# Performance work log

Hardware: AMD Instinct MI355X
Metric: run time of the kernel (lower is better)

The kernel has to match this reference:

```python
import jax, jax.numpy as jnp
import numpy as np
import math

B, S, D, H = 2048, 32, 1024, 16
DK = D // H
EPS = 1e-5

def setup_inputs() -> dict:
    key = jax.random.key(0)
    ks = jax.random.split(key, 8)
    w_scale = 0.02  # realistic init scale for linear weights
    # Weights stored as (d_in, d_out): y = x @ W + b (same math as torch x @ W.T)
    return {
        "x":  jax.random.normal(ks[0], (B, S, D), jnp.float32),
        "ln_g": jnp.ones((D,), jnp.float32),
        "ln_b": jnp.zeros((D,), jnp.float32),
        "wq": jax.random.normal(ks[1], (D, D), jnp.float32) * w_scale,
        "bq": jnp.zeros((D,), jnp.float32),
        "wk": jax.random.normal(ks[2], (D, D), jnp.float32) * w_scale,
        "bk": jnp.zeros((D,), jnp.float32),
        "wv": jax.random.normal(ks[3], (D, D), jnp.float32) * w_scale,
        "bv": jnp.zeros((D,), jnp.float32),
        "wo": jax.random.normal(ks[4], (D, D), jnp.float32) * w_scale,
        "bo": jnp.zeros((D,), jnp.float32),
        "rel_bias": jax.random.normal(ks[5], (H, 32, 32), jnp.float32),
    }

def reference(x, ln_g, ln_b, wq, bq, wk, bk, wv, bv, wo, bo, rel_bias):
    b, s, d = x.shape
    h = rel_bias.shape[0]
    dk = d // h
    residual = x
    # LayerNorm (eps=1e-5)
    mu = jnp.mean(x, axis=-1, keepdims=True)
    var = jnp.mean(jnp.square(x - mu), axis=-1, keepdims=True)
    xn = (x - mu) * jax.lax.rsqrt(var + EPS) * ln_g + ln_b
    # QKV projections -> [b, h, s, dk]
    def split_heads(t):
        return t.reshape(b, s, h, dk).transpose(0, 2, 1, 3)
    Q = split_heads(xn @ wq + bq)
    K = split_heads(xn @ wk + bk)
    V = split_heads(xn @ wv + bv)
    scores = jnp.einsum('bhqd,bhkd->bhqk', Q, K) / jnp.sqrt(jnp.float32(dk))
    if s <= 32:  # static at trace time, matching the torch branch
        scores = scores + rel_bias[:, :s, :s][None]
    attn = jax.nn.softmax(scores, axis=-1)
    ctx = jnp.einsum('bhqk,bhkd->bhqd', attn, V)
    ctx = ctx.transpose(0, 2, 1, 3).reshape(b, s, d)
    out = ctx @ wo + bo  # dropout is identity in eval
    return residual + out
```

## Files before the change

### kernel.cpp

```cpp
#include <hip/hip_runtime.h>
#include <stdint.h>


typedef __attribute__((ext_vector_type(8))) short bf16x8;
typedef __attribute__((ext_vector_type(4))) float f32x4;
typedef __attribute__((ext_vector_type(16))) float f32x16;

__device__ __forceinline__ float bf2f(unsigned short u) {
    return __uint_as_float(((unsigned)u) << 16);
}
__device__ __forceinline__ unsigned short f2bf(float f) {
    unsigned u = __float_as_uint(f);
    u += 0x7FFFu + ((u >> 16) & 1u);
    return (unsigned short)(u >> 16);
}
__device__ __forceinline__ uint4 pack8(const float* f) {
    uint4 u;
    u.x = (unsigned)f2bf(f[0]) | ((unsigned)f2bf(f[1]) << 16);
    u.y = (unsigned)f2bf(f[2]) | ((unsigned)f2bf(f[3]) << 16);
    u.z = (unsigned)f2bf(f[4]) | ((unsigned)f2bf(f[5]) << 16);
    u.w = (unsigned)f2bf(f[6]) | ((unsigned)f2bf(f[7]) << 16);
    return u;
}

typedef __attribute__((address_space(3))) unsigned lds_u32;
typedef const __attribute__((address_space(1))) unsigned glb_u32;
__device__ __forceinline__ void gld16(const void* g, void* l) {
    __builtin_amdgcn_global_load_lds((glb_u32*)g, (lds_u32*)l, 16, 0, 0);
}

__global__ __launch_bounds__(256) void transpose_w(
    const float* __restrict__ wq, const float* __restrict__ wk,
    const float* __restrict__ wv, const float* __restrict__ wo,
    unsigned short* __restrict__ wcatT, unsigned short* __restrict__ woT)
{
    __shared__ unsigned short T[64 * 72];
    int bid = blockIdx.x;
    int p = bid >> 8;
    int t = bid & 255;
    int k0 = (t >> 4) * 64, n0 = (t & 15) * 64;
    const float* src = (p == 0) ? wq : (p == 1) ? wk : (p == 2) ? wv : wo;
    unsigned short* dst = (p < 3) ? (wcatT + (size_t)p * 1048576) : woT;
    int tid = threadIdx.x;
#pragma unroll
    for (int it = 0; it < 2; it++) {
        int flat = it * 2048 + tid * 8;
        int r = flat >> 6, c = flat & 63;
        const float* s4 = src + (size_t)(k0 + r) * 1024 + n0 + c;
        float4 u0 = *(const float4*)s4;
        float4 u1 = *(const float4*)(s4 + 4);
        float f[8] = {u0.x, u0.y, u0.z, u0.w, u1.x, u1.y, u1.z, u1.w};
        *(uint4*)&T[r * 72 + c] = pack8(f);
    }
    __syncthreads();
#pragma unroll
    for (int it = 0; it < 2; it++) {
        int flat = it * 2048 + tid * 8;
        int rn = flat >> 6, ck = flat & 63;
        unsigned short v[8];
#pragma unroll
        for (int j = 0; j < 8; j++) v[j] = T[(ck + j) * 72 + rn];
        uint4 u;
        u.x = (unsigned)v[0] | ((unsigned)v[1] << 16);
        u.y = (unsigned)v[2] | ((unsigned)v[3] << 16);
        u.z = (unsigned)v[4] | ((unsigned)v[5] << 16);
        u.w = (unsigned)v[6] | ((unsigned)v[7] << 16);
        *(uint4*)(dst + (size_t)(n0 + rn) * 1024 + k0 + ck) = u;
    }
}

__global__ __launch_bounds__(256) void ln_kernel(
    const float* __restrict__ x, const float* __restrict__ gg,
    const float* __restrict__ bb, unsigned short* __restrict__ xn)
{
    int l = threadIdx.x & 63;
    size_t row = (size_t)blockIdx.x * 4 + (threadIdx.x >> 6);
    const float* xr = x + row * 1024;
    float f0[8], f1[8];
    *(float4*)&f0[0] = *(const float4*)(xr + l * 8);
    *(float4*)&f0[4] = *(const float4*)(xr + l * 8 + 4);
    *(float4*)&f1[0] = *(const float4*)(xr + 512 + l * 8);
    *(float4*)&f1[4] = *(const float4*)(xr + 512 + l * 8 + 4);
    float s = 0.f, s2 = 0.f;
#pragma unroll
    for (int j = 0; j < 8; j++) { s += f0[j] + f1[j]; s2 += f0[j] * f0[j] + f1[j] * f1[j]; }
#pragma unroll
    for (int m = 1; m < 64; m <<= 1) { s += __shfl_xor(s, m); s2 += __shfl_xor(s2, m); }
    float mu = s * (1.f / 1024.f);
    float var = s2 * (1.f / 1024.f) - mu * mu;
    float rs = rsqrtf(var + 1e-5f);
    float fg0[8], fg1[8], fb0[8], fb1[8];
    *(float4*)&fg0[0] = *(const float4*)(gg + l * 8);
    *(float4*)&fg0[4] = *(const float4*)(gg + l * 8 + 4);
    *(float4*)&fg1[0] = *(const float4*)(gg + 512 + l * 8);
    *(float4*)&fg1[4] = *(const float4*)(gg + 512 + l * 8 + 4);
    *(float4*)&fb0[0] = *(const float4*)(bb + l * 8);
    *(float4*)&fb0[4] = *(const float4*)(bb + l * 8 + 4);
    *(float4*)&fb1[0] = *(const float4*)(bb + 512 + l * 8);
    *(float4*)&fb1[4] = *(const float4*)(bb + 512 + l * 8 + 4);
    float o0[8], o1[8];
#pragma unroll
    for (int j = 0; j < 8; j++) {
        o0[j] = (f0[j] - mu) * rs * fg0[j] + fb0[j];
        o1[j] = (f1[j] - mu) * rs * fg1[j] + fb1[j];
    }
    *(uint4*)(xn + row * 1024 + l * 8) = pack8(o0);
    *(uint4*)(xn + row * 1024 + 512 + l * 8) = pack8(o1);
}

#define FENCE asm volatile("" ::: "memory")
#define BARRIER do { FENCE; __builtin_amdgcn_s_barrier(); FENCE; } while (0)
#define WAIT_LGKM0 do { asm volatile("s_waitcnt lgkmcnt(0)" ::: "memory"); \
                        __builtin_amdgcn_sched_barrier(0); } while (0)
#define VMCNT(n) asm volatile("s_waitcnt vmcnt(" #n ")" ::: "memory")

#define SAp(buf) (LDSU + (buf) * 16384)
#define SBp(buf) (LDSU + 32768 + (buf) * 16384)

#define STG(gb, h, kcol, ldsreg) do { \
    const unsigned short* _g = (gb) + (size_t)((h) * 128) * 1024 + (kcol); \
    unsigned short* _d = (ldsreg) + ((h) * 128 + w * 8) * 64; \
    gld16(_g, _d); gld16(_g + 64 * 1024, _d + 64 * 64); } while (0)

#define LDA(buf, q, rfq, ks) (*(const bf16x8*)&SAp(buf)[ \
    (wm * 128 + (q) * 32 + (rfq) * 16 + (l & 15)) * 64 + ((((ks) * 32) + khi) ^ aswz)])
#define LDB(buf, cf, ks) (*(const bf16x8*)&SBp(buf)[ \
    (wn * 64 + (cf) * 16 + (l & 15)) * 64 + ((((ks) * 32) + khi) ^ aswz)])

#define MFMA_QUAD(q) do { \
    _Pragma("unroll") \
    for (int cf = 0; cf < 4; cf++) { \
        acc[(q)*2+0][cf] = __builtin_amdgcn_mfma_f32_16x16x32_bf16(aF00, bF[cf][0], acc[(q)*2+0][cf], 0, 0, 0); \
        acc[(q)*2+0][cf] = __builtin_amdgcn_mfma_f32_16x16x32_bf16(aF01, bF[cf][1], acc[(q)*2+0][cf], 0, 0, 0); \
        acc[(q)*2+1][cf] = __builtin_amdgcn_mfma_f32_16x16x32_bf16(aF10, bF[cf][0], acc[(q)*2+1][cf], 0, 0, 0); \
        acc[(q)*2+1][cf] = __builtin_amdgcn_mfma_f32_16x16x32_bf16(aF11, bF[cf][1], acc[(q)*2+1][cf], 0, 0, 0); \
    } } while (0)

#define PHASE(buf, q, STAGE_STMT, TAIL_STMT) do { \
    bf16x8 aF00 = LDA(buf, q, 0, 0), aF01 = LDA(buf, q, 0, 1); \
    bf16x8 aF10 = LDA(buf, q, 1, 0), aF11 = LDA(buf, q, 1, 1); \
    if ((q) == 0) { \
        _Pragma("unroll") \
        for (int cf = 0; cf < 4; cf++) { bF[cf][0] = LDB(buf, cf, 0); bF[cf][1] = LDB(buf, cf, 1); } \
    } \
    STAGE_STMT; \
    BARRIER; \
    WAIT_LGKM0; \
    __builtin_amdgcn_s_setprio(1); \
    MFMA_QUAD(q); \
    __builtin_amdgcn_s_setprio(0); \
    TAIL_STMT; \
    BARRIER; \
} while (0)

template <int MODE>
__global__ __launch_bounds__(512, 2) void gemm8(
    const unsigned short* __restrict__ A, const unsigned short* __restrict__ Bt,
    const float* __restrict__ bz0, const float* __restrict__ bz1,
    const float* __restrict__ bz2, const float* __restrict__ resid,
    void* __restrict__ outv, int NTL, size_t pstride)
{
    __shared__ __align__(16) unsigned short LDSU[65536];
    int cpx = gridDim.x >> 3;
    int bid = (blockIdx.x & 7) * cpx + (blockIdx.x >> 3);
    int mt = bid / NTL, ntl = bid % NTL;
    int m0 = mt * 256, n0 = ntl * 256;
    int tid = threadIdx.x, l = tid & 63, w = tid >> 6;
    int wm = w >> 2, wn = w & 3;
    int khi = (l >> 4) * 8;
    int aswz = (l & 7) * 8;

    const unsigned short* Ag = A + (size_t)(m0 + w * 8 + (l >> 3)) * 1024 + ((l & 7) ^ (l >> 3)) * 8;
    const unsigned short* Bg = Bt + (size_t)(n0 + w * 8 + (l >> 3)) * 1024 + ((l & 7) ^ (l >> 3)) * 8;
    unsigned short* sA0 = SAp(0);
    unsigned short* sA1 = SAp(1);
    unsigned short* sB0 = SBp(0);
    unsigned short* sB1 = SBp(1);

    f32x4 acc[8][4];
#pragma unroll
    for (int i = 0; i < 8; i++)
#pragma unroll
        for (int j = 0; j < 4; j++)
#pragma unroll
            for (int v = 0; v < 4; v++) acc[i][j][v] = 0.f;

    bf16x8 bF[4][2];

    STG(Ag, 0, 0, sA0); STG(Ag, 1, 0, sA0);
    STG(Bg, 0, 0, sB0); STG(Bg, 1, 0, sB0);
    STG(Bg, 0, 64, sB1); STG(Bg, 1, 64, sB1);
    VMCNT(4);
    BARRIER;

    for (int it = 0; it < 7; ++it) {
        int koff = it * 128;
        PHASE(0, 0, STG(Ag, 0, koff + 64, sA1), (void)0);
        PHASE(0, 1, STG(Ag, 1, koff + 64, sA1), (void)0);
        PHASE(0, 2, STG(Bg, 0, koff + 128, sB0), (void)0);
        PHASE(0, 3, STG(Bg, 1, koff + 128, sB0), VMCNT(4));
        PHASE(1, 0, STG(Ag, 0, koff + 128, sA0), (void)0);
        PHASE(1, 1, STG(Ag, 1, koff + 128, sA0), (void)0);
        PHASE(1, 2, STG(Bg, 0, koff + 192, sB1), (void)0);
        PHASE(1, 3, STG(Bg, 1, koff + 192, sB1), VMCNT(4));
    }
    PHASE(0, 0, STG(Ag, 0, 960, sA1), (void)0);
    PHASE(0, 1, STG(Ag, 1, 960, sA1), (void)0);
    PHASE(0, 2, (void)0, (void)0);
    PHASE(0, 3, (void)0, VMCNT(0));
    PHASE(1, 0, (void)0, (void)0);
    PHASE(1, 1, (void)0, (void)0);
    PHASE(1, 2, (void)0, (void)0);
    PHASE(1, 3, (void)0, (void)0);
    __builtin_amdgcn_sched_barrier(0);

    if (MODE == 0) {
        unsigned short* Cs = LDSU;
        unsigned short* out = (unsigned short*)outv;
        int p = n0 >> 10;
        const float* bp = (p == 0) ? bz0 : (p == 1) ? bz1 : bz2;
        size_t pbase = (size_t)p * pstride;
        __syncthreads();
#pragma unroll
        for (int cf = 0; cf < 4; cf++) {
            int colc = wn * 64 + cf * 16 + (l & 15);
            int nn = ((n0 + colc) & 1023);
            float bias = bp[nn];
            int c8 = colc >> 3, ce = colc & 7;
#pragma unroll
            for (int rf = 0; rf < 8; rf++) {
#pragma unroll
                for (int v = 0; v < 4; v++) {
                    int rloc = wm * 128 + rf * 16 + (l >> 4) * 4 + v;
                    Cs[rloc * 256 + ((c8 ^ (rloc & 7)) << 3) + ce] =
                        f2bf(acc[rf][cf][v] + bias);
                }
            }
        }
        __syncthreads();
        int bg0 = m0 >> 5;
        int hg0 = (n0 & 1023) >> 6;
#pragma unroll
        for (int k = 0; k < 4; k++) {
            int pi = w * 4 + k;
            int b = pi >> 2, hh = pi & 3;
#pragma unroll
            for (int r4 = 0; r4 < 4; r4++) {
                int c = r4 * 64 + l;
                int s = c >> 3, d8 = c & 7;
                int row = b * 32 + s;
                int c8 = hh * 8 + d8;
                uint4 val = *(const uint4*)&Cs[row * 256 + ((c8 ^ (row & 7)) << 3)];
                size_t dst = pbase + (((size_t)((bg0 + b) * 16 + hg0 + hh) * 32 + s) << 6) + d8 * 8;
                *(uint4*)(out + dst) = val;
            }
        }
    } else {
        float* Cf = (float*)LDSU;
        float* out = (float*)outv;
        int gcol = n0 + l * 4;
        float4 bzv = *(const float4*)(bz0 + gcol);
#pragma unroll
        for (int pass = 0; pass < 2; pass++) {
            __syncthreads();
#pragma unroll
            for (int rfq = 0; rfq < 4; rfq++) {
                int rf = pass * 4 + rfq;
#pragma unroll
                for (int cf = 0; cf < 4; cf++) {
                    int c0 = wn * 64 + cf * 16 + (l & 15);
                    int c4 = c0 >> 2, ce = c0 & 3;
#pragma unroll
                    for (int v = 0; v < 4; v++) {
                        int rl = wm * 64 + rfq * 16 + (l >> 4) * 4 + v;
                        Cf[rl * 256 + ((c4 ^ (rl & 7)) << 2) + ce] = acc[rf][cf][v];
                    }
                }
            }
            __syncthreads();
#pragma unroll
            for (int rb4 = 0; rb4 < 4; rb4++) {
                float4 rz[4], cv[4];
#pragma unroll
                for (int k = 0; k < 4; k++) {
                    int rr = (rb4 * 4 + k) * 8 + w;
                    int grow = m0 + (rr & 63) + ((rr >> 6) << 7) + pass * 64;
                    rz[k] = *(const float4*)(resid + (size_t)grow * 1024 + gcol);
                }
#pragma unroll
                for (int k = 0; k < 4; k++) {
                    int rr = (rb4 * 4 + k) * 8 + w;
                    cv[k] = *(const float4*)&Cf[rr * 256 + ((l ^ (rr & 7)) << 2)];
                }
#pragma unroll
                for (int k = 0; k < 4; k++) {
                    int rr = (rb4 * 4 + k) * 8 + w;
                    int grow = m0 + (rr & 63) + ((rr >> 6) << 7) + pass * 64;
                    float4 o;
                    o.x = cv[k].x + bzv.x + rz[k].x;
                    o.y = cv[k].y + bzv.y + rz[k].y;
                    o.z = cv[k].z + bzv.z + rz[k].z;
                    o.w = cv[k].w + bzv.w + rz[k].w;
                    *(float4*)(out + (size_t)grow * 1024 + gcol) = o;
                }
            }
        }
    }
}

__global__ __launch_bounds__(512) void attn_kernel(
    const unsigned short* __restrict__ qkv, const float* __restrict__ rb,
    unsigned short* __restrict__ ctx, size_t pstride)
{
    __shared__ unsigned short VT[8][64 * 40];
    __shared__ unsigned short Ps[8][32 * 40];
    int w8 = threadIdx.x >> 6, l = threadIdx.x & 63;
    int col = l & 31, hi = l >> 5;
    int bh = blockIdx.x * 8 + w8, h = bh & 15;
    size_t base = (size_t)bh << 11;
    const unsigned short* Qb = qkv + base;
    const unsigned short* Kb = Qb + pstride;
    const unsigned short* Vb = Kb + pstride;
    unsigned short* vt = VT[w8];
    unsigned short* ps = Ps[w8];

#pragma unroll
    for (int r = 0; r < 4; r++) {
        int flat = r * 512 + l * 8;
        int s = flat >> 6, d0 = flat & 63;
        uint4 u = *(const uint4*)(Vb + flat);
        const unsigned short* e = (const unsigned short*)&u;
#pragma unroll
        for (int j = 0; j < 8; j++) vt[(d0 + j) * 40 + s] = e[j];
    }

    f32x16 acc;
#pragma unroll
    for (int i = 0; i < 16; i++) acc[i] = 0.f;
#pragma unroll
    for (int t = 0; t < 4; t++) {
        bf16x8 aQ = *(const bf16x8*)(Qb + col * 64 + t * 16 + hi * 8);
        bf16x8 bK = *(const bf16x8*)(Kb + col * 64 + t * 16 + hi * 8);
        acc = __builtin_amdgcn_mfma_f32_32x32x16_bf16(aQ, bK, acc, 0, 0, 0);
    }

    const float* rbh = rb + h * 1024;
#pragma unroll
    for (int r = 0; r < 16; r++) {
        int m = (r & 3) + 8 * (r >> 2) + 4 * hi;
        float v = acc[r] * 0.125f + rbh[m * 32 + col];
        float mx = v;
#pragma unroll
        for (int msk = 1; msk < 32; msk <<= 1) mx = fmaxf(mx, __shfl_xor(mx, msk));
        float e = __expf(v - mx);
        float sm = e;
#pragma unroll
        for (int msk = 1; msk < 32; msk <<= 1) sm += __shfl_xor(sm, msk);
        ps[m * 40 + col] = f2bf(e / sm);
    }

    bf16x8 pa0 = *(const bf16x8*)&ps[(l & 31) * 40 + hi * 8];
    bf16x8 pa1 = *(const bf16x8*)&ps[(l & 31) * 40 + 16 + hi * 8];
    size_t rowb = (size_t)(bh >> 4) * 32;
#pragma unroll
    for (int c2 = 0; c2 < 2; c2++) {
        bf16x8 vb0 = *(const bf16x8*)&vt[(c2 * 32 + (l & 31)) * 40 + hi * 8];
        bf16x8 vb1 = *(const bf16x8*)&vt[(c2 * 32 + (l & 31)) * 40 + 16 + hi * 8];
        f32x16 o;
#pragma unroll
        for (int i = 0; i < 16; i++) o[i] = 0.f;
        o = __builtin_amdgcn_mfma_f32_32x32x16_bf16(pa0, vb0, o, 0, 0, 0);
        o = __builtin_amdgcn_mfma_f32_32x32x16_bf16(pa1, vb1, o, 0, 0, 0);
#pragma unroll
        for (int r = 0; r < 16; r++) {
            int m = (r & 3) + 8 * (r >> 2) + 4 * hi;
            ctx[(rowb + m) * 1024 + h * 64 + c2 * 32 + col] = f2bf(o[r]);
        }
    }
}

extern "C" void kernel_launch(void* const* d_in, const int* in_sizes, int n_in,
                              void* d_out, int out_size, void* d_ws, size_t ws_size,
                              hipStream_t stream)
{
    const float* x  = (const float*)d_in[0];
    const float* lg = (const float*)d_in[1];
    const float* lb = (const float*)d_in[2];
    const float* wq = (const float*)d_in[3];
    const float* bq = (const float*)d_in[4];
    const float* wk = (const float*)d_in[5];
    const float* bk = (const float*)d_in[6];
    const float* wv = (const float*)d_in[7];
    const float* bv = (const float*)d_in[8];
    const float* wo = (const float*)d_in[9];
    const float* bo = (const float*)d_in[10];
    const float* rb = (const float*)d_in[11];
    float* out = (float*)d_out;
    unsigned short* ws = (unsigned short*)d_ws;

    unsigned short* wcatT = ws;
    unsigned short* woT   = wcatT + 3145728;
    unsigned short* xnctx = woT + 1048576;
    unsigned short* qkvc  = xnctx + 67108864ull;

    const size_t elems_fixed = 3145728ull + 1048576ull + 67108864ull;
    const size_t need1 = (elems_fixed + 201326592ull) * 2;
    const size_t need4 = (elems_fixed + 50331648ull) * 2;
    int nChunks = (ws_size >= need1) ? 1 : (ws_size >= need4) ? 4 : 8;
    int rowsPer = 65536 / nChunks;
    size_t pstr = (size_t)rowsPer * 1024;

    transpose_w<<<dim3(1024), dim3(256), 0, stream>>>(wq, wk, wv, wo, wcatT, woT);
    ln_kernel<<<dim3(16384), dim3(256), 0, stream>>>(x, lg, lb, xnctx);

    int gemm0Grid = (rowsPer / 256) * 12;
    int attnGrid  = rowsPer / 16;

    for (int c = 0; c < nChunks; c++) {
        const unsigned short* Ac = xnctx + (size_t)c * pstr;
        unsigned short* ctxc = xnctx + (size_t)c * pstr;
        gemm8<0><<<dim3(gemm0Grid), dim3(512), 0, stream>>>(
            Ac, wcatT, bq, bk, bv, (const float*)nullptr, (void*)qkvc, 12, pstr);
        attn_kernel<<<dim3(attnGrid), dim3(512), 0, stream>>>(qkvc, rb, ctxc, pstr);
    }

    gemm8<1><<<dim3(1024), dim3(512), 0, stream>>>(
        xnctx, woT, bo, bo, bo, x, (void*)out, 4, 0);
}
```

Baseline: 785.0 us.

## Fuse QKV projection with per-head attention in one kernel

Replaces the chunked QKV GEMM plus separate attention kernel with one fused kernel. Each block computes a 256-row by 192-column tile (Q, K, V for one head), writes it to LDS with bias, and runs the 32x32 attention per wave directly from LDS. This removes the global round-trip of the QKV intermediate and the chunking logic. In exchange it uses a less efficient 256x192 GEMM tile at one block per CU because of the larger LDS footprint, and xn now re-reads the A tile for every head.

Result: no change. 782.1 us (-0.4%).

```diff
diff --git a/kernel.cpp b/kernel.cpp
--- a/kernel.cpp
+++ b/kernel.cpp
@@ -114,12 +114,180 @@
                         __builtin_amdgcn_sched_barrier(0); } while (0)
 #define VMCNT(n) asm volatile("s_waitcnt vmcnt(" #n ")" ::: "memory")
 
+#define FQ_SA(buf) (LDSU + (buf) * 16384)
+#define FQ_SB(buf) (LDSU + 32768 + (buf) * 12288)
+#define QS_OFF 0
+#define KS_OFF 18432
+#define VT_OFF 36864
+#define PS_OFF 57344
+
+#define ASTG(buf, g, koff) gld16(Ag + (size_t)(g) * 65536 + (koff), FQ_SA(buf) + ((g) * 64 + w * 8) * 64)
+#define BSTG(buf, p, koff) gld16(((p) == 0 ? Bgq : (p) == 1 ? Bgk : Bgv) + (koff), \
+                                 FQ_SB(buf) + ((p) * 64 + w * 8) * 64)
+
+#define FLDA(buf, q, rfq, ks) (*(const bf16x8*)&FQ_SA(buf)[ \
+    (wm * 128 + (q) * 32 + (rfq) * 16 + (l & 15)) * 64 + ((((ks) * 32) + khi) ^ aswz)])
+#define FLDB(buf, cf, ks) (*(const bf16x8*)&FQ_SB(buf)[ \
+    (wn * 48 + (cf) * 16 + (l & 15)) * 64 + ((((ks) * 32) + khi) ^ aswz)])
+
+#define MFMA_TRI(q) do { \
+    _Pragma("unroll") \
+    for (int cf = 0; cf < 3; cf++) { \
+        acc[(q)*2+0][cf] = __builtin_amdgcn_mfma_f32_16x16x32_bf16(aF00, bF[cf][0], acc[(q)*2+0][cf], 0, 0, 0); \
+        acc[(q)*2+0][cf] = __builtin_amdgcn_mfma_f32_16x16x32_bf16(aF01, bF[cf][1], acc[(q)*2+0][cf], 0, 0, 0); \
+        acc[(q)*2+1][cf] = __builtin_amdgcn_mfma_f32_16x16x32_bf16(aF10, bF[cf][0], acc[(q)*2+1][cf], 0, 0, 0); \
+        acc[(q)*2+1][cf] = __builtin_amdgcn_mfma_f32_16x16x32_bf16(aF11, bF[cf][1], acc[(q)*2+1][cf], 0, 0, 0); \
+    } } while (0)
+
+#define FPHASE(buf, q, STAGE_STMT, TAIL_STMT) do { \
+    bf16x8 aF00 = FLDA(buf, q, 0, 0), aF01 = FLDA(buf, q, 0, 1); \
+    bf16x8 aF10 = FLDA(buf, q, 1, 0), aF11 = FLDA(buf, q, 1, 1); \
+    if ((q) == 0) { \
+        _Pragma("unroll") \
+        for (int cf = 0; cf < 3; cf++) { bF[cf][0] = FLDB(buf, cf, 0); bF[cf][1] = FLDB(buf, cf, 1); } \
+    } \
+    STAGE_STMT; \
+    BARRIER; \
+    WAIT_LGKM0; \
+    __builtin_amdgcn_s_setprio(1); \
+    MFMA_TRI(q); \
+    __builtin_amdgcn_s_setprio(0); \
+    TAIL_STMT; \
+    BARRIER; \
+} while (0)
+
+__global__ __launch_bounds__(512, 1) void fqa_kernel(
+    const unsigned short* __restrict__ A, const unsigned short* __restrict__ wcatT,
+    const float* __restrict__ bq, const float* __restrict__ bk,
+    const float* __restrict__ bv, const float* __restrict__ rb,
+    unsigned short* __restrict__ ctx)
+{
+    __shared__ __align__(16) unsigned short LDSU[67584];
+    int cpx = gridDim.x >> 3;
+    int bid = (blockIdx.x & 7) * cpx + (blockIdx.x >> 3);
+    int mp = bid >> 4, h = bid & 15;
+    int m0 = mp * 256;
+    int tid = threadIdx.x, l = tid & 63, w = tid >> 6;
+    int wm = w >> 2, wn = w & 3;
+    int khi = (l >> 4) * 8;
+    int aswz = (l & 7) * 8;
+    int swzc = ((l & 7) ^ (l >> 3)) * 8;
+
+    const unsigned short* Ag  = A + (size_t)(m0 + w * 8 + (l >> 3)) * 1024 + swzc;
+    const unsigned short* Bgq = wcatT + (size_t)(h * 64 + w * 8 + (l >> 3)) * 1024 + swzc;
+    const unsigned short* Bgk = Bgq + 1048576ull;
+    const unsigned short* Bgv = Bgq + 2097152ull;
+
+    f32x4 acc[8][3];
+#pragma unroll
+    for (int i = 0; i < 8; i++)
+#pragma unroll
+        for (int j = 0; j < 3; j++)
+#pragma unroll
+            for (int v = 0; v < 4; v++) acc[i][j][v] = 0.f;
+
+    bf16x8 bF[3][2];
+
+    ASTG(0, 0, 0); ASTG(0, 1, 0); ASTG(0, 2, 0); ASTG(0, 3, 0);
+    BSTG(0, 0, 0); BSTG(0, 1, 0); BSTG(0, 2, 0);
+    BSTG(1, 0, 64); BSTG(1, 1, 64); BSTG(1, 2, 64);
+    VMCNT(3);
+    BARRIER;
+
+    for (int it = 0; it < 7; ++it) {
+        int ko1 = (2 * it + 1) * 64, ko2 = (2 * it + 2) * 64, ko3 = (2 * it + 3) * 64;
+        FPHASE(0, 0, do { ASTG(1, 0, ko1); ASTG(1, 1, ko1); } while (0), (void)0);
+        FPHASE(0, 1, do { ASTG(1, 2, ko1); ASTG(1, 3, ko1); } while (0), (void)0);
+        FPHASE(0, 2, do { BSTG(0, 0, ko2); BSTG(0, 1, ko2); } while (0), (void)0);
+        FPHASE(0, 3, BSTG(0, 2, ko2), VMCNT(3));
+        FPHASE(1, 0, do { ASTG(0, 0, ko2); ASTG(0, 1, ko2); } while (0), (void)0);
+        FPHASE(1, 1, do { ASTG(0, 2, ko2); ASTG(0, 3, ko2); } while (0), (void)0);
+        FPHASE(1, 2, do { BSTG(1, 0, ko3); BSTG(1, 1, ko3); } while (0), (void)0);
+        FPHASE(1, 3, BSTG(1, 2, ko3), VMCNT(3));
+    }
+    FPHASE(0, 0, do { ASTG(1, 0, 960); ASTG(1, 1, 960); } while (0), (void)0);
+    FPHASE(0, 1, do { ASTG(1, 2, 960); ASTG(1, 3, 960); } while (0), (void)0);
+    FPHASE(0, 2, (void)0, (void)0);
+    FPHASE(0, 3, (void)0, VMCNT(0));
+    FPHASE(1, 0, (void)0, (void)0);
+    FPHASE(1, 1, (void)0, (void)0);
+    FPHASE(1, 2, (void)0, (void)0);
+    FPHASE(1, 3, (void)0, (void)0);
+    __builtin_amdgcn_sched_barrier(0);
+
+#pragma unroll
+    for (int cf = 0; cf < 3; cf++) {
+        int seg = (wn * 3 + cf) >> 2;
+        int cseg = wn * 48 + cf * 16 + (l & 15) - (seg << 6);
+        const float* bp = (seg == 0) ? bq : (seg == 1) ? bk : bv;
+        float bias = bp[h * 64 + cseg];
+#pragma unroll
+        for (int ai = 0; ai < 8; ai++) {
+#pragma unroll
+            for (int v = 0; v < 4; v++) {
+                int row = wm * 128 + ai * 16 + (l >> 4) * 4 + v;
+                unsigned short val = f2bf(acc[ai][cf][v] + bias);
+                if (seg == 0)      LDSU[QS_OFF + row * 72 + cseg] = val;
+                else if (seg == 1) LDSU[KS_OFF + row * 72 + cseg] = val;
+                else               LDSU[VT_OFF + (((row >> 5) << 6) + cseg) * 40 + (row & 31)] = val;
+            }
+        }
+    }
+    __syncthreads();
+
+    {
+        int col = l & 31, hi = l >> 5;
+        f32x16 s;
+#pragma unroll
+        for (int i = 0; i < 16; i++) s[i] = 0.f;
+#pragma unroll
+        for (int t = 0; t < 4; t++) {
+            bf16x8 aQ = *(const bf16x8*)&LDSU[QS_OFF + (w * 32 + col) * 72 + t * 16 + hi * 8];
+            bf16x8 bK = *(const bf16x8*)&LDSU[KS_OFF + (w * 32 + col) * 72 + t * 16 + hi * 8];
+            s = __builtin_amdgcn_mfma_f32_32x32x16_bf16(aQ, bK, s, 0, 0, 0);
+        }
+        const float* rbh = rb + h * 1024;
+        unsigned short* ps = LDSU + PS_OFF + w * 1280;
+#pragma unroll
+        for (int r = 0; r < 16; r++) {
+            int m = (r & 3) + 8 * (r >> 2) + 4 * hi;
+            float v = s[r] * 0.125f + rbh[m * 32 + col];
+            float mx = v;
+#pragma unroll
+            for (int msk = 1; msk < 32; msk <<= 1) mx = fmaxf(mx, __shfl_xor(mx, msk));
+            float e = __expf(v - mx);
+            float sm = e;
+#pragma unroll
+            for (int msk = 1; msk < 32; msk <<= 1) sm += __shfl_xor(sm, msk);
+            ps[m * 40 + col] = f2bf(e / sm);
+        }
+        bf16x8 pa0 = *(const bf16x8*)&ps[col * 40 + hi * 8];
+        bf16x8 pa1 = *(const bf16x8*)&ps[col * 40 + 16 + hi * 8];
+        size_t rowb = ((size_t)mp * 8 + w) * 32;
+#pragma unroll
+        for (int c2 = 0; c2 < 2; c2++) {
+            bf16x8 vb0 = *(const bf16x8*)&LDSU[VT_OFF + (w * 64 + c2 * 32 + col) * 40 + hi * 8];
+            bf16x8 vb1 = *(const bf16x8*)&LDSU[VT_OFF + (w * 64 + c2 * 32 + col) * 40 + 16 + hi * 8];
+            f32x16 o;
+#pragma unroll
+            for (int i = 0; i < 16; i++) o[i] = 0.f;
+            o = __builtin_amdgcn_mfma_f32_32x32x16_bf16(pa0, vb0, o, 0, 0, 0);
+            o = __builtin_amdgcn_mfma_f32_32x32x16_bf16(pa1, vb1, o, 0, 0, 0);
+#pragma unroll
+            for (int r = 0; r < 16; r++) {
+                int m = (r & 3) + 8 * (r >> 2) + 4 * hi;
+                ctx[(rowb + m) * 1024 + h * 64 + c2 * 32 + col] = f2bf(o[r]);
+            }
+        }
+    }
+}
+
 #define SAp(buf) (LDSU + (buf) * 16384)
 #define SBp(buf) (LDSU + 32768 + (buf) * 16384)
 
-#define STG(gb, h, kcol, ldsreg) do { \
-    const unsigned short* _g = (gb) + (size_t)((h) * 128) * 1024 + (kcol); \
-    unsigned short* _d = (ldsreg) + ((h) * 128 + w * 8) * 64; \
+#define STG(gb, hh, kcol, ldsreg) do { \
+    const unsigned short* _g = (gb) + (size_t)((hh) * 128) * 1024 + (kcol); \
+    unsigned short* _d = (ldsreg) + ((hh) * 128 + w * 8) * 64; \
     gld16(_g, _d); gld16(_g + 64 * 1024, _d + 64 * 64); } while (0)
 
 #define LDA(buf, q, rfq, ks) (*(const bf16x8*)&SAp(buf)[ \
@@ -153,12 +321,10 @@
     BARRIER; \
 } while (0)
 
-template <int MODE>
-__global__ __launch_bounds__(512, 2) void gemm8(
+__global__ __launch_bounds__(512, 2) void gemm8res(
     const unsigned short* __restrict__ A, const unsigned short* __restrict__ Bt,
-    const float* __restrict__ bz0, const float* __restrict__ bz1,
-    const float* __restrict__ bz2, const float* __restrict__ resid,
-    void* __restrict__ outv, int NTL, size_t pstride)
+    const float* __restrict__ bz0, const float* __restrict__ resid,
+    float* __restrict__ out, int NTL)
 {
     __shared__ __align__(16) unsigned short LDSU[65536];
     int cpx = gridDim.x >> 3;
@@ -214,167 +380,52 @@
     PHASE(1, 3, (void)0, (void)0);
     __builtin_amdgcn_sched_barrier(0);
 
-    if (MODE == 0) {
-        unsigned short* Cs = LDSU;
-        unsigned short* out = (unsigned short*)outv;
-        int p = n0 >> 10;
-        const float* bp = (p == 0) ? bz0 : (p == 1) ? bz1 : bz2;
-        size_t pbase = (size_t)p * pstride;
+    float* Cf = (float*)LDSU;
+    int gcol = n0 + l * 4;
+    float4 bzv = *(const float4*)(bz0 + gcol);
+#pragma unroll
+    for (int pass = 0; pass < 2; pass++) {
         __syncthreads();
 #pragma unroll
-        for (int cf = 0; cf < 4; cf++) {
-            int colc = wn * 64 + cf * 16 + (l & 15);
-            int nn = ((n0 + colc) & 1023);
-            float bias = bp[nn];
-            int c8 = colc >> 3, ce = colc & 7;
-#pragma unroll
-            for (int rf = 0; rf < 8; rf++) {
+        for (int rfq = 0; rfq < 4; rfq++) {
+            int rf = pass * 4 + rfq;
+#pragma unroll
+            for (int cf = 0; cf < 4; cf++) {
+                int c0 = wn * 64 + cf * 16 + (l & 15);
+                int c4 = c0 >> 2, ce = c0 & 3;
 #pragma unroll
                 for (int v = 0; v < 4; v++) {
-                    int rloc = wm * 128 + rf * 16 + (l >> 4) * 4 + v;
-                    Cs[rloc * 256 + ((c8 ^ (rloc & 7)) << 3) + ce] =
-                        f2bf(acc[rf][cf][v] + bias);
+                    int rl = wm * 64 + rfq * 16 + (l >> 4) * 4 + v;
+                    Cf[rl * 256 + ((c4 ^ (rl & 7)) << 2) + ce] = acc[rf][cf][v];
                 }
             }
         }
         __syncthreads();
-        int bg0 = m0 >> 5;
-        int hg0 = (n0 & 1023) >> 6;
-#pragma unroll
-        for (int k = 0; k < 4; k++) {
-            int pi = w * 4 + k;
-            int b = pi >> 2, hh = pi & 3;
-#pragma unroll
-            for (int r4 = 0; r4 < 4; r4++) {
-                int c = r4 * 64 + l;
-                int s = c >> 3, d8 = c & 7;
-                int row = b * 32 + s;
-                int c8 = hh * 8 + d8;
-                uint4 val = *(const uint4*)&Cs[row * 256 + ((c8 ^ (row & 7)) << 3)];
-                size_t dst = pbase + (((size_t)((bg0 + b) * 16 + hg0 + hh) * 32 + s) << 6) + d8 * 8;
-                *(uint4*)(out + dst) = val;
-            }
-        }
-    } else {
-        float* Cf = (float*)LDSU;
-        float* out = (float*)outv;
-        int gcol = n0 + l * 4;
-        float4 bzv = *(const float4*)(bz0 + gcol);
-#pragma unroll
-        for (int pass = 0; pass < 2; pass++) {
-            __syncthreads();
-#pragma unroll
-            for (int rfq = 0; rfq < 4; rfq++) {
-                int rf = pass * 4 + rfq;
-#pragma unroll
-                for (int cf = 0; cf < 4; cf++) {
-                    int c0 = wn * 64 + cf * 16 + (l & 15);
-                    int c4 = c0 >> 2, ce = c0 & 3;
-#pragma unroll
-                    for (int v = 0; v < 4; v++) {
-                        int rl = wm * 64 + rfq * 16 + (l >> 4) * 4 + v;
-                        Cf[rl * 256 + ((c4 ^ (rl & 7)) << 2) + ce] = acc[rf][cf][v];
-                    }
-                }
-            }
-            __syncthreads();
-#pragma unroll
-            for (int rb4 = 0; rb4 < 4; rb4++) {
-                float4 rz[4], cv[4];
-#pragma unroll
-                for (int k = 0; k < 4; k++) {
-                    int rr = (rb4 * 4 + k) * 8 + w;
-                    int grow = m0 + (rr & 63) + ((rr >> 6) << 7) + pass * 64;
-                    rz[k] = *(const float4*)(resid + (size_t)grow * 1024 + gcol);
-                }
-#pragma unroll
-                for (int k = 0; k < 4; k++) {
-                    int rr = (rb4 * 4 + k) * 8 + w;
-                    cv[k] = *(const float4*)&Cf[rr * 256 + ((l ^ (rr & 7)) << 2)];
-                }
-#pragma unroll
-                for (int k = 0; k < 4; k++) {
-                    int rr = (rb4 * 4 + k) * 8 + w;
-                    int grow = m0 + (rr & 63) + ((rr >> 6) << 7) + pass * 64;
-                    float4 o;
-                    o.x = cv[k].x + bzv.x + rz[k].x;
-                    o.y = cv[k].y + bzv.y + rz[k].y;
-                    o.z = cv[k].z + bzv.z + rz[k].z;
-                    o.w = cv[k].w + bzv.w + rz[k].w;
-                    *(float4*)(out + (size_t)grow * 1024 + gcol) = o;
-                }
-            }
-        }
-    }
-}
-
-__global__ __launch_bounds__(512) void attn_kernel(
-    const unsigned short* __restrict__ qkv, const float* __restrict__ rb,
-    unsigned short* __restrict__ ctx, size_t pstride)
-{
-    __shared__ unsigned short VT[8][64 * 40];
-    __shared__ unsigned short Ps[8][32 * 40];
-    int w8 = threadIdx.x >> 6, l = threadIdx.x & 63;
-    int col = l & 31, hi = l >> 5;
-    int bh = blockIdx.x * 8 + w8, h = bh & 15;
-    size_t base = (size_t)bh << 11;
-    const unsigned short* Qb = qkv + base;
-    const unsigned short* Kb = Qb + pstride;
-    const unsigned short* Vb = Kb + pstride;
-    unsigned short* vt = VT[w8];
-    unsigned short* ps = Ps[w8];
-
-#pragma unroll
-    for (int r = 0; r < 4; r++) {
-        int flat = r * 512 + l * 8;
-        int s = flat >> 6, d0 = flat & 63;
-        uint4 u = *(const uint4*)(Vb + flat);
-        const unsigned short* e = (const unsigned short*)&u;
-#pragma unroll
-        for (int j = 0; j < 8; j++) vt[(d0 + j) * 40 + s] = e[j];
-    }
-
-    f32x16 acc;
-#pragma unroll
-    for (int i = 0; i < 16; i++) acc[i] = 0.f;
-#pragma unroll
-    for (int t = 0; t < 4; t++) {
-        bf16x8 aQ = *(const bf16x8*)(Qb + col * 64 + t * 16 + hi * 8);
-        bf16x8 bK = *(const bf16x8*)(Kb + col * 64 + t * 16 + hi * 8);
-        acc = __builtin_amdgcn_mfma_f32_32x32x16_bf16(aQ, bK, acc, 0, 0, 0);
-    }
-
-    const float* rbh = rb + h * 1024;
-#pragma unroll
-    for (int r = 0; r < 16; r++) {
-        int m = (r & 3) + 8 * (r >> 2) + 4 * hi;
-        float v = acc[r] * 0.125f + rbh[m * 32 + col];
-        float mx = v;
-#pragma unroll
-        for (int msk = 1; msk < 32; msk <<= 1) mx = fmaxf(mx, __shfl_xor(mx, msk));
-        float e = __expf(v - mx);
-        float sm = e;
-#pragma unroll
-        for (int msk = 1; msk < 32; msk <<= 1) sm += __shfl_xor(sm, msk);
-        ps[m * 40 + col] = f2bf(e / sm);
-    }
-
-    bf16x8 pa0 = *(const bf16x8*)&ps[(l & 31) * 40 + hi * 8];
-    bf16x8 pa1 = *(const bf16x8*)&ps[(l & 31) * 40 + 16 + hi * 8];
-    size_t rowb = (size_t)(bh >> 4) * 32;
-#pragma unroll
-    for (int c2 = 0; c2 < 2; c2++) {
-        bf16x8 vb0 = *(const bf16x8*)&vt[(c2 * 32 + (l & 31)) * 40 + hi * 8];
-        bf16x8 vb1 = *(const bf16x8*)&vt[(c2 * 32 + (l & 31)) * 40 + 16 + hi * 8];
-        f32x16 o;
-#pragma unroll
-        for (int i = 0; i < 16; i++) o[i] = 0.f;
-        o = __builtin_amdgcn_mfma_f32_32x32x16_bf16(pa0, vb0, o, 0, 0, 0);
-        o = __builtin_amdgcn_mfma_f32_32x32x16_bf16(pa1, vb1, o, 0, 0, 0);
-#pragma unroll
-        for (int r = 0; r < 16; r++) {
-            int m = (r & 3) + 8 * (r >> 2) + 4 * hi;
-            ctx[(rowb + m) * 1024 + h * 64 + c2 * 32 + col] = f2bf(o[r]);
+#pragma unroll
+        for (int rb4 = 0; rb4 < 4; rb4++) {
+            float4 rz[4], cv[4];
+#pragma unroll
+            for (int k = 0; k < 4; k++) {
+                int rr = (rb4 * 4 + k) * 8 + w;
+                int grow = m0 + (rr & 63) + ((rr >> 6) << 7) + pass * 64;
+                rz[k] = *(const float4*)(resid + (size_t)grow * 1024 + gcol);
+            }
+#pragma unroll
+            for (int k = 0; k < 4; k++) {
+                int rr = (rb4 * 4 + k) * 8 + w;
+                cv[k] = *(const float4*)&Cf[rr * 256 + ((l ^ (rr & 7)) << 2)];
+            }
+#pragma unroll
+            for (int k = 0; k < 4; k++) {
+                int rr = (rb4 * 4 + k) * 8 + w;
+                int grow = m0 + (rr & 63) + ((rr >> 6) << 7) + pass * 64;
+                float4 o;
+                o.x = cv[k].x + bzv.x + rz[k].x;
+                o.y = cv[k].y + bzv.y + rz[k].y;
+                o.z = cv[k].z + bzv.z + rz[k].z;
+                o.w = cv[k].w + bzv.w + rz[k].w;
+                *(float4*)(out + (size_t)grow * 1024 + gcol) = o;
+            }
         }
     }
 }
@@ -400,30 +451,13 @@
 
     unsigned short* wcatT = ws;
     unsigned short* woT   = wcatT + 3145728;
-    unsigned short* xnctx = woT + 1048576;
-    unsigned short* qkvc  = xnctx + 67108864ull;
-
-    const size_t elems_fixed = 3145728ull + 1048576ull + 67108864ull;
-    const size_t need1 = (elems_fixed + 201326592ull) * 2;
-    const size_t need4 = (elems_fixed + 50331648ull) * 2;
-    int nChunks = (ws_size >= need1) ? 1 : (ws_size >= need4) ? 4 : 8;
-    int rowsPer = 65536 / nChunks;
-    size_t pstr = (size_t)rowsPer * 1024;
+    unsigned short* xn    = woT + 1048576;
+    unsigned short* ctx   = xn + 67108864ull;
 
     transpose_w<<<dim3(1024), dim3(256), 0, stream>>>(wq, wk, wv, wo, wcatT, woT);
-    ln_kernel<<<dim3(16384), dim3(256), 0, stream>>>(x, lg, lb, xnctx);
-
-    int gemm0Grid = (rowsPer / 256) * 12;
-    int attnGrid  = rowsPer / 16;
-
-    for (int c = 0; c < nChunks; c++) {
-        const unsigned short* Ac = xnctx + (size_t)c * pstr;
-        unsigned short* ctxc = xnctx + (size_t)c * pstr;
-        gemm8<0><<<dim3(gemm0Grid), dim3(512), 0, stream>>>(
-            Ac, wcatT, bq, bk, bv, (const float*)nullptr, (void*)qkvc, 12, pstr);
-        attn_kernel<<<dim3(attnGrid), dim3(512), 0, stream>>>(qkvc, rb, ctxc, pstr);
-    }
-
-    gemm8<1><<<dim3(1024), dim3(512), 0, stream>>>(
-        xnctx, woT, bo, bo, bo, x, (void*)out, 4, 0);
-}
+    ln_kernel<<<dim3(16384), dim3(256), 0, stream>>>(x, lg, lb, xn);
+
+    fqa_kernel<<<dim3(4096), dim3(512), 0, stream>>>(xn, wcatT, bq, bk, bv, rb, ctx);
+
+    gemm8res<<<dim3(1024), dim3(512), 0, stream>>>(ctx, woT, bo, x, out, 4);
+}
```

## Swap GEMM tile order to N-major and stage attention output through LDS

Applied to the files above, without the earlier changes.

The GEMM block index now maps with the M tile varying fastest, so concurrently running blocks share the same weight N-tile while walking down rows of A. In the attention kernel, both PV MFMAs are issued together and the results are written into LDS (reusing the V buffer) instead of going straight to global memory as scattered 2-byte stores. They are then copied out as 16-byte row-contiguous stores to ctx. This targets poor store coalescing in attention and L2 reuse in the GEMMs, at the cost of an extra LDS round trip and a possible race if the vt buffer is overwritten while other lanes are still reading it without a barrier.

Measured after the change: 830.1 us. 5.8% more time.

```diff
diff --git a/kernel.cpp b/kernel.cpp
--- a/kernel.cpp
+++ b/kernel.cpp
@@ -117,9 +117,9 @@
 #define SAp(buf) (LDSU + (buf) * 16384)
 #define SBp(buf) (LDSU + 32768 + (buf) * 16384)
 
-#define STG(gb, h, kcol, ldsreg) do { \
-    const unsigned short* _g = (gb) + (size_t)((h) * 128) * 1024 + (kcol); \
-    unsigned short* _d = (ldsreg) + ((h) * 128 + w * 8) * 64; \
+#define STG(gb, hh, kcol, ldsreg) do { \
+    const unsigned short* _g = (gb) + (size_t)((hh) * 128) * 1024 + (kcol); \
+    unsigned short* _d = (ldsreg) + ((hh) * 128 + w * 8) * 64; \
     gld16(_g, _d); gld16(_g + 64 * 1024, _d + 64 * 64); } while (0)
 
 #define LDA(buf, q, rfq, ks) (*(const bf16x8*)&SAp(buf)[ \
@@ -158,12 +158,12 @@
     const unsigned short* __restrict__ A, const unsigned short* __restrict__ Bt,
     const float* __restrict__ bz0, const float* __restrict__ bz1,
     const float* __restrict__ bz2, const float* __restrict__ resid,
-    void* __restrict__ outv, int NTL, size_t pstride)
+    void* __restrict__ outv, int MT, size_t pstride)
 {
     __shared__ __align__(16) unsigned short LDSU[65536];
     int cpx = gridDim.x >> 3;
     int bid = (blockIdx.x & 7) * cpx + (blockIdx.x >> 3);
-    int mt = bid / NTL, ntl = bid % NTL;
+    int ntl = bid / MT, mt = bid % MT;
     int m0 = mt * 256, n0 = ntl * 256;
     int tid = threadIdx.x, l = tid & 63, w = tid >> 6;
     int wm = w >> 2, wn = w & 3;
@@ -359,23 +359,33 @@
         ps[m * 40 + col] = f2bf(e / sm);
     }
 
-    bf16x8 pa0 = *(const bf16x8*)&ps[(l & 31) * 40 + hi * 8];
-    bf16x8 pa1 = *(const bf16x8*)&ps[(l & 31) * 40 + 16 + hi * 8];
+    bf16x8 pa0 = *(const bf16x8*)&ps[col * 40 + hi * 8];
+    bf16x8 pa1 = *(const bf16x8*)&ps[col * 40 + 16 + hi * 8];
+    bf16x8 vb00 = *(const bf16x8*)&vt[(col) * 40 + hi * 8];
+    bf16x8 vb01 = *(const bf16x8*)&vt[(col) * 40 + 16 + hi * 8];
+    bf16x8 vb10 = *(const bf16x8*)&vt[(32 + col) * 40 + hi * 8];
+    bf16x8 vb11 = *(const bf16x8*)&vt[(32 + col) * 40 + 16 + hi * 8];
+    f32x16 o0, o1;
+#pragma unroll
+    for (int i = 0; i < 16; i++) { o0[i] = 0.f; o1[i] = 0.f; }
+    o0 = __builtin_amdgcn_mfma_f32_32x32x16_bf16(pa0, vb00, o0, 0, 0, 0);
+    o0 = __builtin_amdgcn_mfma_f32_32x32x16_bf16(pa1, vb01, o0, 0, 0, 0);
+    o1 = __builtin_amdgcn_mfma_f32_32x32x16_bf16(pa0, vb10, o1, 0, 0, 0);
+    o1 = __builtin_amdgcn_mfma_f32_32x32x16_bf16(pa1, vb11, o1, 0, 0, 0);
+
+#pragma unroll
+    for (int r = 0; r < 16; r++) {
+        int m = (r & 3) + 8 * (r >> 2) + 4 * hi;
+        vt[m * 72 + col]      = f2bf(o0[r]);
+        vt[m * 72 + 32 + col] = f2bf(o1[r]);
+    }
     size_t rowb = (size_t)(bh >> 4) * 32;
 #pragma unroll
-    for (int c2 = 0; c2 < 2; c2++) {
-        bf16x8 vb0 = *(const bf16x8*)&vt[(c2 * 32 + (l & 31)) * 40 + hi * 8];
-        bf16x8 vb1 = *(const bf16x8*)&vt[(c2 * 32 + (l & 31)) * 40 + 16 + hi * 8];
-        f32x16 o;
-#pragma unroll
-        for (int i = 0; i < 16; i++) o[i] = 0.f;
-        o = __builtin_amdgcn_mfma_f32_32x32x16_bf16(pa0, vb0, o, 0, 0, 0);
-        o = __builtin_amdgcn_mfma_f32_32x32x16_bf16(pa1, vb1, o, 0, 0, 0);
-#pragma unroll
-        for (int r = 0; r < 16; r++) {
-            int m = (r & 3) + 8 * (r >> 2) + 4 * hi;
-            ctx[(rowb + m) * 1024 + h * 64 + c2 * 32 + col] = f2bf(o[r]);
-        }
+    for (int pass = 0; pass < 4; pass++) {
+        int row = pass * 8 + (l >> 3);
+        int c = (l & 7) * 8;
+        uint4 val = *(const uint4*)&vt[row * 72 + c];
+        *(uint4*)(ctx + (rowb + row) * 1024 + h * 64 + c) = val;
     }
 }
 
@@ -409,21 +419,22 @@
     int nChunks = (ws_size >= need1) ? 1 : (ws_size >= need4) ? 4 : 8;
     int rowsPer = 65536 / nChunks;
     size_t pstr = (size_t)rowsPer * 1024;
+    int MT0 = rowsPer / 256;
 
     transpose_w<<<dim3(1024), dim3(256), 0, stream>>>(wq, wk, wv, wo, wcatT, woT);
     ln_kernel<<<dim3(16384), dim3(256), 0, stream>>>(x, lg, lb, xnctx);
 
-    int gemm0Grid = (rowsPer / 256) * 12;
+    int gemm0Grid = MT0 * 12;
     int attnGrid  = rowsPer / 16;
 
     for (int c = 0; c < nChunks; c++) {
         const unsigned short* Ac = xnctx + (size_t)c * pstr;
         unsigned short* ctxc = xnctx + (size_t)c * pstr;
         gemm8<0><<<dim3(gemm0Grid), dim3(512), 0, stream>>>(
-            Ac, wcatT, bq, bk, bv, (const float*)nullptr, (void*)qkvc, 12, pstr);
+            Ac, wcatT, bq, bk, bv, (const float*)nullptr, (void*)qkvc, MT0, pstr);
         attn_kernel<<<dim3(attnGrid), dim3(512), 0, stream>>>(qkvc, rb, ctxc, pstr);
     }
 
     gemm8<1><<<dim3(1024), dim3(512), 0, stream>>>(
-        xnctx, woT, bo, bo, bo, x, (void*)out, 4, 0);
-}
+        xnctx, woT, bo, bo, bo, x, (void*)out, 256, 0);
+}
```
